# Optimization experiments

Measured on AMD Instinct MI355X. Metric: run time of the kernel, lower is better.

## Reference

```python
import jax, jax.numpy as jnp
from jax import lax
import numpy as np

B, S, E = 512, 128, 300
NF = 100          # filters per kernel size
NUM_CLASSES = 5


def setup_inputs() -> dict:
    key = jax.random.key(0)
    ks = jax.random.split(key, 9)
    def w(k, shape, fan_in):
        bound = 1.0 / np.sqrt(fan_in)
        return jax.random.uniform(k, shape, jnp.float32, -bound, bound)
    return {
        "x":   jax.random.normal(ks[0], (B, 1, S, E), jnp.float32),
        # conv weights: [out_ch=NF, in_ch=1, kh, kw=E] (the 100 separate 1-channel
        # convs of each kernel size are stacked into one grouped weight tensor)
        "w3": w(ks[1], (NF, 1, 3, E), 3 * E),
        "b3": w(ks[2], (NF,), 3 * E),
        "w4": w(ks[3], (NF, 1, 4, E), 4 * E),
        "b4": w(ks[4], (NF,), 4 * E),
        "w5": w(ks[5], (NF, 1, 5, E), 5 * E),
        "b5": w(ks[6], (NF,), 5 * E),
        "Wfc": w(ks[7], (NUM_CLASSES, 3 * NF), 3 * NF),
        "bfc": w(ks[8], (NUM_CLASSES,), 3 * NF),
    }


def _branch(x, w, b, pad):
    # conv over [B,1,S,E] with kernel [NF,1,k,E]; width fully consumed -> out [B,NF,S',1]
    y = lax.conv_general_dilated(
        x, w, window_strides=(1, 1), padding=[(pad, pad), (0, 0)],
        dimension_numbers=("NCHW", "OIHW", "NCHW"))
    y = jax.nn.relu(y + b[None, :, None, None])
    # relu then global max-pool over the length dim == max over (S', 1)
    return jnp.max(y, axis=(2, 3))  # [B, NF]


def reference(x, w3, b3, w4, b4, w5, b5, Wfc, bfc):
    feats = jnp.concatenate(
        [_branch(x, w3, b3, 0),   # k=3, no padding
         _branch(x, w4, b4, 1),   # k=4, padding (1,0)
         _branch(x, w5, b5, 2)],  # k=5, padding (2,0)
        axis=1)                   # [B, 300]
    logits = feats @ Wfc.T + bfc  # dropout is identity in eval mode
    return jax.nn.log_softmax(logits, axis=1)
```

## Files before the change

kernel.cpp:

```cpp
#include <hip/hip_runtime.h>

typedef __bf16 bf16x8 __attribute__((ext_vector_type(8)));
typedef float  f32x4  __attribute__((ext_vector_type(4)));
typedef unsigned short u16;

#define NB    512
#define SEQ   128
#define EMB   300
#define NT_TOT 19
#define KT_TOT 50
#define KT_BYTES (NT_TOT * 1024)
#define WU_ELEMS (304 * 1600)
#define OFF_FEATS (WU_ELEMS * 2)

#define AROW 656
#define A_BYTES (69 * AROW)

__device__ __forceinline__ u16 f2bf(float f) {
  unsigned u = __builtin_bit_cast(unsigned, f);
  return (u16)((u + 0x7fffu + ((u >> 16) & 1u)) >> 16);
}

__global__ void prep_weights(const float* __restrict__ w3, const float* __restrict__ w4,
                             const float* __restrict__ w5, u16* __restrict__ wu) {
  int idx = blockIdx.x * blockDim.x + threadIdx.x;
  if (idx >= WU_ELEMS) return;
  int j = idx & 7, l = (idx >> 3) & 63, t = idx >> 9;
  int nt = t % NT_TOT, kt = t / NT_TOT;
  int f  = nt * 16 + (l & 15);
  int kk = kt * 32 + ((l >> 4) << 3) + j;
  int dk = kk / 320, e = kk - dk * 320;
  float v = 0.f;
  if (f < 300 && e < 300) {
    if (f < 100)      { if (dk >= 2) v = w3[(f * 3 + dk - 2) * 300 + e]; }
    else if (f < 200) { if (dk >= 1) v = w4[((f - 100) * 4 + dk - 1) * 300 + e]; }
    else              {              v = w5[((f - 200) * 5 + dk) * 300 + e]; }
  }
  wu[idx] = f2bf(v);
}

template<int NTW>
__device__ __forceinline__ void kloop_epi(const char* xs, const char* wB,
                                          int ntb, int l, int b, int s0,
                                          const float* __restrict__ b3,
                                          const float* __restrict__ b4,
                                          const float* __restrict__ b5,
                                          float* __restrict__ feats) {
  const int lo = l & 15, hi = l >> 4;

  f32x4 acc[4][NTW];
  #pragma unroll
  for (int mt = 0; mt < 4; ++mt)
    #pragma unroll
    for (int j = 0; j < NTW; ++j) acc[mt][j] = (f32x4){0.f, 0.f, 0.f, 0.f};

  bf16x8 aC[4], aN[4], bC[NTW], bN[NTW];

  const char* gB = wB + ntb * 1024 + l * 16;
  #pragma unroll
  for (int j = 0; j < NTW; ++j) bC[j] = *reinterpret_cast<const bf16x8*>(gB + j * 1024);
  #pragma unroll
  for (int j = 0; j < NTW; ++j) bN[j] = *reinterpret_cast<const bf16x8*>(gB + KT_BYTES + j * 1024);
  gB += 2 * KT_BYTES;

  int abase[4];
  #pragma unroll
  for (int mt = 0; mt < 4; ++mt) abase[mt] = (mt * 16 + lo) * AROW + hi * 16;

  #pragma unroll
  for (int mt = 0; mt < 4; ++mt)
    aC[mt] = *reinterpret_cast<const bf16x8*>(xs + abase[mt]);

#define STEP(AOFF, Acon, Anex, Bcon) {                                         \
    _Pragma("unroll") for (int mt = 0; mt < 4; ++mt)                           \
      Anex[mt] = *reinterpret_cast<const bf16x8*>(xs + abase[mt] + (AOFF));    \
    __builtin_amdgcn_s_setprio(1);                                             \
    _Pragma("unroll") for (int mt = 0; mt < 4; ++mt)                           \
    _Pragma("unroll") for (int j = 0; j < NTW; ++j)                            \
      acc[mt][j] = __builtin_amdgcn_mfma_f32_16x16x32_bf16(Acon[mt], Bcon[j],  \
                                                           acc[mt][j], 0, 0, 0); \
    __builtin_amdgcn_s_setprio(0);                                             \
    _Pragma("unroll") for (int j = 0; j < NTW; ++j)                            \
      Bcon[j] = *reinterpret_cast<const bf16x8*>(gB + j * 1024);               \
    gB += KT_BYTES; }

  #pragma unroll 1
  for (int dk = 0; dk < 5; ++dk) {
    STEP( 64, aC, aN, bC)
    STEP(128, aN, aC, bN)
    STEP(192, aC, aN, bC)
    STEP(256, aN, aC, bN)
    STEP(320, aC, aN, bC)
    STEP(384, aN, aC, bN)
    STEP(448, aC, aN, bC)
    STEP(512, aN, aC, bN)
    STEP(576, aC, aN, bC)
    STEP(656, aN, aC, bN)
    #pragma unroll
    for (int mt = 0; mt < 4; ++mt) abase[mt] += AROW;
  }
#undef STEP

  #pragma unroll
  for (int j = 0; j < NTW; ++j) {
    int f = (ntb + j) * 16 + lo;
    if (f < 300) {
      float bia  = (f < 100) ? b3[f] : (f < 200) ? b4[f - 100] : b5[f - 200];
      int   sval = (f < 100) ? 126   : (f < 200) ? 127         : 128;
      float cmax = 0.f;
      #pragma unroll
      for (int mt = 0; mt < 4; ++mt)
        #pragma unroll
        for (int ii = 0; ii < 4; ++ii) {
          int s = s0 + mt * 16 + hi * 4 + ii;
          float v = acc[mt][j][ii] + bia;
          if (s < sval) cmax = fmaxf(cmax, v);
        }
      cmax = fmaxf(cmax, __shfl_xor(cmax, 16));
      cmax = fmaxf(cmax, __shfl_xor(cmax, 32));
      if (hi == 0)
        atomicMax((int*)&feats[b * 300 + f], __float_as_int(fmaxf(cmax, 0.f)));
    }
  }
}

__global__ __launch_bounds__(256, 2)
void conv_max_kernel(const float* __restrict__ x, const u16* __restrict__ wu,
                     const float* __restrict__ b3, const float* __restrict__ b4,
                     const float* __restrict__ b5, float* __restrict__ feats) {
  __shared__ __align__(16) char xs[A_BYTES];
  const int bid = blockIdx.x;
  const int b = bid >> 1, s0 = (bid & 1) * 64;
  const int tid = threadIdx.x;
  const int l = tid & 63, w = tid >> 6;
  const float* xb = x + (size_t)b * (SEQ * EMB);
  const char*  wB = (const char*)wu;

  for (int t = tid; t < 68 * 80; t += 256) {
    int r = t / 80, cg = t - r * 80;
    int xr = s0 - 2 + r;
    float4 v = make_float4(0.f, 0.f, 0.f, 0.f);
    if (xr >= 0 && xr < SEQ && cg < 75)
      v = *reinterpret_cast<const float4*>(xb + xr * EMB + cg * 4);
    ushort4 h;
    h.x = f2bf(v.x); h.y = f2bf(v.y); h.z = f2bf(v.z); h.w = f2bf(v.w);
    *reinterpret_cast<ushort4*>(xs + r * AROW + cg * 8) = h;
  }
  __syncthreads();

  if (w == 3) kloop_epi<4>(xs, wB, 15, l, b, s0, b3, b4, b5, feats);
  else        kloop_epi<5>(xs, wB, w * 5, l, b, s0, b3, b4, b5, feats);
}

__global__ void fc_kernel(const float* __restrict__ feats, const float* __restrict__ Wfc,
                          const float* __restrict__ bfc, float* __restrict__ out) {
  const int b = blockIdx.x, l = threadIdx.x;
  float acc[5] = {0.f, 0.f, 0.f, 0.f, 0.f};
  for (int e = l; e < 300; e += 64) {
    float fv = feats[b * 300 + e];
    #pragma unroll
    for (int c = 0; c < 5; ++c) acc[c] += fv * Wfc[c * 300 + e];
  }
  #pragma unroll
  for (int off = 32; off; off >>= 1) {
    #pragma unroll
    for (int c = 0; c < 5; ++c) acc[c] += __shfl_down(acc[c], off);
  }
  if (l == 0) {
    float lg[5], m = -1e30f;
    #pragma unroll
    for (int c = 0; c < 5; ++c) { lg[c] = acc[c] + bfc[c]; m = fmaxf(m, lg[c]); }
    float se = 0.f;
    #pragma unroll
    for (int c = 0; c < 5; ++c) se += expf(lg[c] - m);
    float ls = logf(se);
    #pragma unroll
    for (int c = 0; c < 5; ++c) out[b * 5 + c] = lg[c] - m - ls;
  }
}

extern "C" void kernel_launch(void* const* d_in, const int* in_sizes, int n_in,
                              void* d_out, int out_size, void* d_ws, size_t ws_size,
                              hipStream_t stream) {
  const float* x   = (const float*)d_in[0];
  const float* w3  = (const float*)d_in[1];
  const float* b3  = (const float*)d_in[2];
  const float* w4  = (const float*)d_in[3];
  const float* b4  = (const float*)d_in[4];
  const float* w5  = (const float*)d_in[5];
  const float* b5  = (const float*)d_in[6];
  const float* Wfc = (const float*)d_in[7];
  const float* bfc = (const float*)d_in[8];
  float* out = (float*)d_out;

  u16*   wu    = (u16*)d_ws;
  float* feats = (float*)((char*)d_ws + OFF_FEATS);

  hipMemsetAsync(feats, 0, NB * 300 * sizeof(float), stream);

  prep_weights<<<(WU_ELEMS + 255) / 256, 256, 0, stream>>>(w3, w4, w5, wu);
  conv_max_kernel<<<NB * 2, 256, 0, stream>>>(x, wu, b3, b4, b5, feats);
  fc_kernel<<<NB, 64, 0, stream>>>(feats, Wfc, bfc, out);
}
```

Before: 75.83 us.

## Swizzle LDS input tile with XOR pattern and raise occupancy to three blocks

Replaces the padded LDS row stride (656 bytes) with an unpadded 640-byte stride and an XOR swizzle on 16-byte chunks keyed by row index. The same swizzle is applied on the staging stores and on the MFMA A-fragment loads. This keeps bank-conflict avoidance while shrinking shared memory per block. Launch bounds are raised to allow three blocks per CU, which may increase register pressure or spilling.

```diff
diff --git a/kernel.cpp b/kernel.cpp
--- a/kernel.cpp
+++ b/kernel.cpp
@@ -13,7 +13,7 @@
 #define WU_ELEMS (304 * 1600)
 #define OFF_FEATS (WU_ELEMS * 2)
 
-#define AROW 656
+#define AROW 640
 #define A_BYTES (69 * AROW)
 
 __device__ __forceinline__ u16 f2bf(float f) {
@@ -67,13 +67,16 @@
   #pragma unroll
   for (int mt = 0; mt < 4; ++mt) abase[mt] = (mt * 16 + lo) * AROW + hi * 16;
 
-  #pragma unroll
-  for (int mt = 0; mt < 4; ++mt)
-    aC[mt] = *reinterpret_cast<const bf16x8*>(xs + abase[mt]);
-
-#define STEP(AOFF, Acon, Anex, Bcon) {                                         \
+  {
+    const int sw = (lo & 7) << 4;
+    #pragma unroll
+    for (int mt = 0; mt < 4; ++mt)
+      aC[mt] = *reinterpret_cast<const bf16x8*>(xs + (abase[mt] ^ sw));
+  }
+
+#define STEP(AOFF, SW, Acon, Anex, Bcon) {                                     \
     _Pragma("unroll") for (int mt = 0; mt < 4; ++mt)                           \
-      Anex[mt] = *reinterpret_cast<const bf16x8*>(xs + abase[mt] + (AOFF));    \
+      Anex[mt] = *reinterpret_cast<const bf16x8*>(xs + ((abase[mt] + (AOFF)) ^ (SW))); \
     __builtin_amdgcn_s_setprio(1);                                             \
     _Pragma("unroll") for (int mt = 0; mt < 4; ++mt)                           \
     _Pragma("unroll") for (int j = 0; j < NTW; ++j)                            \
@@ -86,16 +89,18 @@
 
   #pragma unroll 1
   for (int dk = 0; dk < 5; ++dk) {
-    STEP( 64, aC, aN, bC)
-    STEP(128, aN, aC, bN)
-    STEP(192, aC, aN, bC)
-    STEP(256, aN, aC, bN)
-    STEP(320, aC, aN, bC)
-    STEP(384, aN, aC, bN)
-    STEP(448, aC, aN, bC)
-    STEP(512, aN, aC, bN)
-    STEP(576, aC, aN, bC)
-    STEP(656, aN, aC, bN)
+    const int sw0 = ((lo + dk) & 7) << 4;
+    const int sw1 = ((lo + dk + 1) & 7) << 4;
+    STEP( 64, sw0, aC, aN, bC)
+    STEP(128, sw0, aN, aC, bN)
+    STEP(192, sw0, aC, aN, bC)
+    STEP(256, sw0, aN, aC, bN)
+    STEP(320, sw0, aC, aN, bC)
+    STEP(384, sw0, aN, aC, bN)
+    STEP(448, sw0, aC, aN, bC)
+    STEP(512, sw0, aN, aC, bN)
+    STEP(576, sw0, aC, aN, bC)
+    STEP(640, sw1, aN, aC, bN)
     #pragma unroll
     for (int mt = 0; mt < 4; ++mt) abase[mt] += AROW;
   }
@@ -124,7 +129,7 @@
   }
 }
 
-__global__ __launch_bounds__(256, 2)
+__global__ __launch_bounds__(256, 3)
 void conv_max_kernel(const float* __restrict__ x, const u16* __restrict__ wu,
                      const float* __restrict__ b3, const float* __restrict__ b4,
                      const float* __restrict__ b5, float* __restrict__ feats) {
@@ -144,7 +149,8 @@
       v = *reinterpret_cast<const float4*>(xb + xr * EMB + cg * 4);
     ushort4 h;
     h.x = f2bf(v.x); h.y = f2bf(v.y); h.z = f2bf(v.z); h.w = f2bf(v.w);
-    *reinterpret_cast<ushort4*>(xs + r * AROW + cg * 8) = h;
+    int boff = (r * AROW + cg * 8) ^ ((r & 7) << 4);
+    *reinterpret_cast<ushort4*>(xs + boff) = h;
   }
   __syncthreads();
 
```

Measured after the change: 77.15 us. No clear change (+1.7%).

## Skip zero-padded taps by splitting filter tiles per kernel height

Applied to the files above, without the earlier changes.

The old path ran every filter tile across all five tap rows, so the k=3 and k=4 filters spent MFMAs on zero-padded weight rows. Each kernel height now gets its own packed weight stream, and the tap loop runs only 3, 4 or 5 rows, with filter tiles rebalanced across the four waves. Total MFMA work and weight traffic fall. The cost is more template instantiations, more register buffers for the four-deep B prefetch, possible wave imbalance, and hardcoded byte offsets into the packed stream.

```diff
diff --git a/kernel.cpp b/kernel.cpp
--- a/kernel.cpp
+++ b/kernel.cpp
@@ -7,14 +7,12 @@
 #define NB    512
 #define SEQ   128
 #define EMB   300
-#define NT_TOT 19
-#define KT_TOT 50
-#define KT_BYTES (NT_TOT * 1024)
-#define WU_ELEMS (304 * 1600)
-#define OFF_FEATS (WU_ELEMS * 2)
 
 #define AROW 656
 #define A_BYTES (69 * AROW)
+
+#define PREP_TOT 430080
+#define OFF_FEATS 876544
 
 __device__ __forceinline__ u16 f2bf(float f) {
   unsigned u = __builtin_bit_cast(unsigned, f);
@@ -24,29 +22,37 @@
 __global__ void prep_weights(const float* __restrict__ w3, const float* __restrict__ w4,
                              const float* __restrict__ w5, u16* __restrict__ wu) {
   int idx = blockIdx.x * blockDim.x + threadIdx.x;
-  if (idx >= WU_ELEMS) return;
-  int j = idx & 7, l = (idx >> 3) & 63, t = idx >> 9;
-  int nt = t % NT_TOT, kt = t / NT_TOT;
-  int f  = nt * 16 + (l & 15);
+  if (idx >= PREP_TOT) return;
+  const int cum[8]  = {0, 61440, 107520, 189440, 215040, 276480, 327680, 430080};
+  const int ntwA[7] = {4, 3, 4, 1, 3, 2, 4};
+  const int khA[7]  = {3, 3, 4, 5, 4, 5, 5};
+  const int fl0A[7] = {0, 64, 0, 0, 64, 16, 48};
+  int p = 0;
+  #pragma unroll
+  for (int q = 0; q < 6; ++q) if (idx >= cum[q + 1]) p = q + 1;
+  int rem = idx - cum[p];
+  int ntw = ntwA[p], kh = khA[p];
+  int j = rem & 7, l = (rem >> 3) & 63, t = rem >> 9;
+  int tloc = t % ntw, kt = t / ntw;
+  int fl = fl0A[p] + tloc * 16 + (l & 15);
   int kk = kt * 32 + ((l >> 4) << 3) + j;
   int dk = kk / 320, e = kk - dk * 320;
   float v = 0.f;
-  if (f < 300 && e < 300) {
-    if (f < 100)      { if (dk >= 2) v = w3[(f * 3 + dk - 2) * 300 + e]; }
-    else if (f < 200) { if (dk >= 1) v = w4[((f - 100) * 4 + dk - 1) * 300 + e]; }
-    else              {              v = w5[((f - 200) * 5 + dk) * 300 + e]; }
+  if (fl < 100 && e < 300) {
+    if (kh == 3)      v = w3[(fl * 3 + dk) * 300 + e];
+    else if (kh == 4) v = w4[(fl * 4 + dk) * 300 + e];
+    else              v = w5[(fl * 5 + dk) * 300 + e];
   }
   wu[idx] = f2bf(v);
 }
 
-template<int NTW>
-__device__ __forceinline__ void kloop_epi(const char* xs, const char* wB,
-                                          int ntb, int l, int b, int s0,
-                                          const float* __restrict__ b3,
-                                          const float* __restrict__ b4,
-                                          const float* __restrict__ b5,
-                                          float* __restrict__ feats) {
+template<int NTW, int KH>
+__device__ __forceinline__ void kloop_epi(const char* xs, const char* gstream,
+                                          int l, int s0, int fl0,
+                                          const float* __restrict__ bias, int sval,
+                                          int foff, int b, float* __restrict__ feats) {
   const int lo = l & 15, hi = l >> 4;
+  constexpr int DK0 = 5 - KH;
 
   f32x4 acc[4][NTW];
   #pragma unroll
@@ -54,59 +60,63 @@
     #pragma unroll
     for (int j = 0; j < NTW; ++j) acc[mt][j] = (f32x4){0.f, 0.f, 0.f, 0.f};
 
-  bf16x8 aC[4], aN[4], bC[NTW], bN[NTW];
-
-  const char* gB = wB + ntb * 1024 + l * 16;
-  #pragma unroll
-  for (int j = 0; j < NTW; ++j) bC[j] = *reinterpret_cast<const bf16x8*>(gB + j * 1024);
-  #pragma unroll
-  for (int j = 0; j < NTW; ++j) bN[j] = *reinterpret_cast<const bf16x8*>(gB + KT_BYTES + j * 1024);
-  gB += 2 * KT_BYTES;
+  bf16x8 aC[4], aN[4], b0[NTW], b1[NTW], b2[NTW], b3s[NTW];
+
+  const char* gB = gstream + l * 16;
+  #pragma unroll
+  for (int j = 0; j < NTW; ++j) b0[j]  = *reinterpret_cast<const bf16x8*>(gB + j * 1024);
+  gB += NTW * 1024;
+  #pragma unroll
+  for (int j = 0; j < NTW; ++j) b1[j]  = *reinterpret_cast<const bf16x8*>(gB + j * 1024);
+  gB += NTW * 1024;
+  #pragma unroll
+  for (int j = 0; j < NTW; ++j) b2[j]  = *reinterpret_cast<const bf16x8*>(gB + j * 1024);
+  gB += NTW * 1024;
+  #pragma unroll
+  for (int j = 0; j < NTW; ++j) b3s[j] = *reinterpret_cast<const bf16x8*>(gB + j * 1024);
+  gB += NTW * 1024;
 
   int abase[4];
   #pragma unroll
-  for (int mt = 0; mt < 4; ++mt) abase[mt] = (mt * 16 + lo) * AROW + hi * 16;
+  for (int mt = 0; mt < 4; ++mt) abase[mt] = (mt * 16 + lo + DK0) * AROW + hi * 16;
 
   #pragma unroll
   for (int mt = 0; mt < 4; ++mt)
     aC[mt] = *reinterpret_cast<const bf16x8*>(xs + abase[mt]);
 
-#define STEP(AOFF, Acon, Anex, Bcon) {                                         \
+#define STEP(AOFF, ACON, ANEX, BSET) {                                         \
     _Pragma("unroll") for (int mt = 0; mt < 4; ++mt)                           \
-      Anex[mt] = *reinterpret_cast<const bf16x8*>(xs + abase[mt] + (AOFF));    \
+      ANEX[mt] = *reinterpret_cast<const bf16x8*>(xs + abase[mt] + (AOFF));    \
     __builtin_amdgcn_s_setprio(1);                                             \
     _Pragma("unroll") for (int mt = 0; mt < 4; ++mt)                           \
     _Pragma("unroll") for (int j = 0; j < NTW; ++j)                            \
-      acc[mt][j] = __builtin_amdgcn_mfma_f32_16x16x32_bf16(Acon[mt], Bcon[j],  \
+      acc[mt][j] = __builtin_amdgcn_mfma_f32_16x16x32_bf16(ACON[mt], BSET[j],  \
                                                            acc[mt][j], 0, 0, 0); \
     __builtin_amdgcn_s_setprio(0);                                             \
     _Pragma("unroll") for (int j = 0; j < NTW; ++j)                            \
-      Bcon[j] = *reinterpret_cast<const bf16x8*>(gB + j * 1024);               \
-    gB += KT_BYTES; }
-
-  #pragma unroll 1
-  for (int dk = 0; dk < 5; ++dk) {
-    STEP( 64, aC, aN, bC)
-    STEP(128, aN, aC, bN)
-    STEP(192, aC, aN, bC)
-    STEP(256, aN, aC, bN)
-    STEP(320, aC, aN, bC)
-    STEP(384, aN, aC, bN)
-    STEP(448, aC, aN, bC)
-    STEP(512, aN, aC, bN)
-    STEP(576, aC, aN, bC)
-    STEP(656, aN, aC, bN)
-    #pragma unroll
-    for (int mt = 0; mt < 4; ++mt) abase[mt] += AROW;
-  }
+      BSET[j] = *reinterpret_cast<const bf16x8*>(gB + j * 1024);               \
+    gB += NTW * 1024; }
+
+#define BODY(SA, SB, SC, SD) {                                                 \
+    STEP( 64, aC, aN, SA) STEP(128, aN, aC, SB) STEP(192, aC, aN, SC)          \
+    STEP(256, aN, aC, SD) STEP(320, aC, aN, SA) STEP(384, aN, aC, SB)          \
+    STEP(448, aC, aN, SC) STEP(512, aN, aC, SD) STEP(576, aC, aN, SA)          \
+    STEP(656, aN, aC, SB)                                                      \
+    _Pragma("unroll") for (int mt = 0; mt < 4; ++mt) abase[mt] += AROW; }
+
+  BODY(b0, b1, b2, b3s)
+  BODY(b2, b3s, b0, b1)
+  BODY(b0, b1, b2, b3s)
+  if constexpr (KH >= 4) { BODY(b2, b3s, b0, b1) }
+  if constexpr (KH == 5) { BODY(b0, b1, b2, b3s) }
+#undef BODY
 #undef STEP
 
   #pragma unroll
   for (int j = 0; j < NTW; ++j) {
-    int f = (ntb + j) * 16 + lo;
-    if (f < 300) {
-      float bia  = (f < 100) ? b3[f] : (f < 200) ? b4[f - 100] : b5[f - 200];
-      int   sval = (f < 100) ? 126   : (f < 200) ? 127         : 128;
+    int fl = fl0 + j * 16 + lo;
+    if (fl < 100) {
+      float bia  = bias[fl];
       float cmax = 0.f;
       #pragma unroll
       for (int mt = 0; mt < 4; ++mt)
@@ -119,7 +129,7 @@
       cmax = fmaxf(cmax, __shfl_xor(cmax, 16));
       cmax = fmaxf(cmax, __shfl_xor(cmax, 32));
       if (hi == 0)
-        atomicMax((int*)&feats[b * 300 + f], __float_as_int(fmaxf(cmax, 0.f)));
+        atomicMax((int*)&feats[b * 300 + foff + fl], __float_as_int(fmaxf(cmax, 0.f)));
     }
   }
 }
@@ -148,8 +158,18 @@
   }
   __syncthreads();
 
-  if (w == 3) kloop_epi<4>(xs, wB, 15, l, b, s0, b3, b4, b5, feats);
-  else        kloop_epi<5>(xs, wB, w * 5, l, b, s0, b3, b4, b5, feats);
+  if (w == 0) {
+    kloop_epi<4, 3>(xs, wB + 0,      l, s0,  0, b3, 126,   0, b, feats);
+    kloop_epi<3, 3>(xs, wB + 122880, l, s0, 64, b3, 126,   0, b, feats);
+  } else if (w == 1) {
+    kloop_epi<4, 4>(xs, wB + 215040, l, s0,  0, b4, 127, 100, b, feats);
+    kloop_epi<1, 5>(xs, wB + 378880, l, s0,  0, b5, 128, 200, b, feats);
+  } else if (w == 2) {
+    kloop_epi<3, 4>(xs, wB + 430080, l, s0, 64, b4, 127, 100, b, feats);
+    kloop_epi<2, 5>(xs, wB + 552960, l, s0, 16, b5, 128, 200, b, feats);
+  } else {
+    kloop_epi<4, 5>(xs, wB + 655360, l, s0, 48, b5, 128, 200, b, feats);
+  }
 }
 
 __global__ void fc_kernel(const float* __restrict__ feats, const float* __restrict__ Wfc,
@@ -198,7 +218,7 @@
 
   hipMemsetAsync(feats, 0, NB * 300 * sizeof(float), stream);
 
-  prep_weights<<<(WU_ELEMS + 255) / 256, 256, 0, stream>>>(w3, w4, w5, wu);
+  prep_weights<<<(PREP_TOT + 255) / 256, 256, 0, stream>>>(w3, w4, w5, wu);
   conv_max_kernel<<<NB * 2, 256, 0, stream>>>(x, wu, b3, b4, b5, feats);
   fc_kernel<<<NB, 64, 0, stream>>>(feats, Wfc, bfc, out);
 }
```

Result: no change. 75.20 us (-0.8%).
